# Performance work log

Measured on AMD Instinct MI355X. Metric: run time of the kernel, lower is better.

Reference implementation:

```python
import jax, jax.numpy as jnp
import numpy as np

NUM_HEADS = 4
GROUPS = 8
EPS = 1e-5


def setup_inputs() -> dict:
    key = jax.random.key(0)
    ks = jax.random.split(key, 8)
    B, C, H, W = 8, 512, 64, 64
    L, E = 77, 768
    std = 0.02
    return {
        "x": jax.random.normal(ks[0], (B, C, H, W), jnp.float32),
        "text_emb": jax.random.normal(ks[1], (B, L, E), jnp.float32),
        "attention_mask": jax.random.randint(ks[2], (B, L), 0, 2, jnp.int32),
        "Wq_w": jax.random.normal(ks[3], (C, C), jnp.float32) * std,
        "Wq_b": jnp.zeros((C,), jnp.float32),
        "Wk_w": jax.random.normal(ks[4], (C, E), jnp.float32) * std,
        "Wk_b": jnp.zeros((C,), jnp.float32),
        "Wv_w": jax.random.normal(ks[5], (C, E), jnp.float32) * std,
        "Wv_b": jnp.zeros((C,), jnp.float32),
        "gn_scale": jnp.ones((C,), jnp.float32),
        "gn_bias": jnp.zeros((C,), jnp.float32),
    }


def reference(x, text_emb, attention_mask, Wq_w, Wq_b, Wk_w, Wk_b, Wv_w, Wv_b, gn_scale, gn_bias):
    B, C, H, W = x.shape
    dh = C // NUM_HEADS
    scale = dh ** -0.5

    # [B, HW, C] queries from image features
    x_flat = x.reshape(B, C, H * W).transpose(0, 2, 1)
    Q = x_flat @ Wq_w.T + Wq_b                 # [B, S, C]
    K = text_emb @ Wk_w.T + Wk_b               # [B, L, C]
    V = text_emb @ Wv_w.T + Wv_b               # [B, L, C]

    def split_heads(t):
        Bt, T, _ = t.shape
        return t.reshape(Bt, T, NUM_HEADS, dh).transpose(0, 2, 1, 3)  # [B, h, T, dh]

    Qh, Kh, Vh = split_heads(Q), split_heads(K), split_heads(V)

    scores = jnp.einsum("bhqd,bhkd->bhqk", Qh, Kh) * scale  # [B, h, S, L]
    mask = (attention_mask == 0)[:, None, None, :]
    scores = jnp.where(mask, -jnp.inf, scores)
    probs = jax.nn.softmax(scores, axis=-1)
    # dropout layers are identity in eval mode
    attn = jnp.einsum("bhqk,bhkd->bhqd", probs, Vh)          # [B, h, S, dh]

    out = attn.transpose(0, 2, 1, 3).reshape(B, H * W, C)    # [B, S, C]
    out = out.transpose(0, 2, 1).reshape(B, C, H, W)

    # GroupNorm(8 groups, affine) over (C/G, H, W) per group
    g = out.reshape(B, GROUPS, -1)
    mean = g.mean(axis=-1, keepdims=True)
    var = g.var(axis=-1, keepdims=True)
    g = (g - mean) * jax.lax.rsqrt(var + EPS)
    out = g.reshape(B, C, H, W) * gn_scale[None, :, None, None] + gn_bias[None, :, None, None]
    return out
```

## Files before the change

### kernel.cpp

```cpp
#include <hip/hip_runtime.h>
#include <hip/hip_bf16.h>
#include <cstdint>


typedef __attribute__((ext_vector_type(8))) short short8;
typedef __attribute__((ext_vector_type(4))) short short4v;
typedef __attribute__((ext_vector_type(4))) float f32x4;

#define DEV __device__ __forceinline__

DEV float bf2f(unsigned short u){ union{uint32_t i; float f;} x; x.i = ((uint32_t)u) << 16; return x.f; }
DEV unsigned short f2bf(float f){ __hip_bfloat16 h = __float2bfloat16(f); return *reinterpret_cast<unsigned short*>(&h); }
DEV short8 ld8(const unsigned short* p){ return *reinterpret_cast<const short8*>(p); }
DEV f32x4 ldf4(const float* p){ return *reinterpret_cast<const f32x4*>(p); }

#if defined(__has_builtin)
#if __has_builtin(__builtin_amdgcn_global_load_lds)
#define HAVE_ASYNC_LDS 1
#endif
#endif

__global__ __launch_bounds__(256) void k_fat(const float* __restrict__ x,
                                             unsigned short* __restrict__ xTt,
                                             const float* __restrict__ text,
                                             const float* __restrict__ Wk,
                                             const float* __restrict__ Wkb,
                                             const float* __restrict__ Wv,
                                             const float* __restrict__ Wvb,
                                             unsigned short* __restrict__ wsK,
                                             unsigned short* __restrict__ wsVt,
                                             const float* __restrict__ Wq,
                                             unsigned short* __restrict__ wsWqT,
                                             int b0, int s_base, int slen, int SB){
  __shared__ unsigned short U[16896];
  const int tid = threadIdx.x;
  const int bx = blockIdx.x, by = blockIdx.y, bz = blockIdx.z;
  const int bg = b0 + bz;
  const int NT = slen >> 8;

  if (bx < NT){
    const int cc = by, c0 = cc * 64;
    const int s0 = s_base + bx * 256;
    {
      const int r = tid >> 2, sub = tid & 3;
      const float* src = &x[((size_t)(bg * 512 + c0 + r)) * 4096 + s0 + sub * 64];
      unsigned short* drow = &U[r * 264 + sub * 64];
      #pragma unroll
      for (int i = 0; i < 8; ++i){
        f32x4 a = ldf4(src + i * 8), b = ldf4(src + i * 8 + 4);
        short8 v;
        #pragma unroll
        for (int j = 0; j < 4; ++j){ v[j] = (short)f2bf(a[j]); v[j + 4] = (short)f2bf(b[j]); }
        *reinterpret_cast<short8*>(drow + i * 8) = v;
      }
    }
    __syncthreads();
    {
      const int j = tid;
      unsigned short v[64];
      #pragma unroll
      for (int r = 0; r < 64; ++r) v[r] = U[r * 264 + j];
      const int sloc = bx * 256 + j;
      unsigned short* dst = &xTt[(((size_t)bz * 8 + cc) * slen + sloc) * 64];
      #pragma unroll
      for (int g = 0; g < 8; ++g)
        *reinterpret_cast<short8*>(dst + g * 8) = *reinterpret_cast<short8*>(&v[g * 8]);
    }
  } else if (bx < NT + 2){
    unsigned short* At = U;
    unsigned short* Bt = U + 5760;
    const int wave = tid >> 6, lane = tid & 63;
    const int m16 = lane & 15, quad = lane >> 4;
    const int uc = (bx - NT) * 8 + by;
    const int u0 = uc * 64;
    const bool isK = (u0 < 512);
    const float* W  = isK ? Wk  : Wv;
    const float* Wb = isK ? Wkb : Wvb;
    const int c0 = u0 & 511;
    const int c  = c0 + wave * 16 + m16;
    f32x4 acc[5];
    #pragma unroll
    for (int mt = 0; mt < 5; ++mt) acc[mt] = (f32x4){0.f, 0.f, 0.f, 0.f};
    for (int kc = 0; kc < 12; ++kc){
      const int e0 = kc * 64;
      #pragma unroll
      for (int it = 0; it < 9; ++it){
        int slot = tid + it * 256;
        if (slot < 1280){
          int row = slot >> 4, e4 = (slot & 15) * 4;
          f32x4 v = (row < 77) ? ldf4(&text[((size_t)(bg * 77 + row)) * 768 + e0 + e4])
                               : (f32x4){0.f, 0.f, 0.f, 0.f};
          short4v o;
          #pragma unroll
          for (int j = 0; j < 4; ++j) o[j] = (short)f2bf(v[j]);
          *reinterpret_cast<short4v*>(&At[row * 72 + e4]) = o;
        } else {
          int bs = slot - 1280;
          int row = bs >> 4, e4 = (bs & 15) * 4;
          f32x4 v = ldf4(&W[((size_t)(c0 + row)) * 768 + e0 + e4]);
          short4v o;
          #pragma unroll
          for (int j = 0; j < 4; ++j) o[j] = (short)f2bf(v[j]);
          *reinterpret_cast<short4v*>(&Bt[row * 72 + e4]) = o;
        }
      }
      __syncthreads();
      #pragma unroll
      for (int kk = 0; kk < 64; kk += 32){
        short8 bf_ = *reinterpret_cast<const short8*>(&Bt[(wave * 16 + m16) * 72 + kk + quad * 8]);
        #pragma unroll
        for (int mt = 0; mt < 5; ++mt){
          short8 af_ = *reinterpret_cast<const short8*>(&At[(mt * 16 + m16) * 72 + kk + quad * 8]);
          acc[mt] = __builtin_amdgcn_mfma_f32_16x16x32_bf16(af_, bf_, acc[mt], 0, 0, 0);
        }
      }
      __syncthreads();
    }
    const float bias = Wb[c];
    if (isK){
      #pragma unroll
      for (int mt = 0; mt < 5; ++mt)
        #pragma unroll
        for (int r = 0; r < 4; ++r){
          int l = mt * 16 + quad * 4 + r;
          if (l < 77) wsK[((size_t)(bz * 77 + l)) * 512 + c] = f2bf(acc[mt][r] + bias);
        }
    } else {
      unsigned short* vr = &wsVt[((size_t)(bz * 512 + c)) * 96];
      #pragma unroll
      for (int mt = 0; mt < 5; ++mt){
        short4v pk;
        #pragma unroll
        for (int r = 0; r < 4; ++r) pk[r] = (short)f2bf(acc[mt][r] + bias);
        *reinterpret_cast<short4v*>(&vr[mt * 16 + quad * 4]) = pk;
      }
      short4v z = {};
      *reinterpret_cast<short4v*>(&vr[80 + quad * 4]) = z;
    }
  } else {
    unsigned short* t = U;
    const int nb = 8 * SB;
    const int p  = by + bz * 8;
    for (int tile = p; tile < 64; tile += nb){
      const int ti = tile >> 3, tj = tile & 7;
      #pragma unroll
      for (int it = 0; it < 2; ++it){
        int slot = tid + it * 256;
        int r = slot >> 3, sg = slot & 7;
        int sw = sg ^ (r >> 3);
        const float* src = &Wq[((size_t)(tj * 64 + r)) * 512 + ti * 64 + sg * 8];
        f32x4 a = ldf4(src), b2 = ldf4(src + 4);
        short8 v;
        #pragma unroll
        for (int j = 0; j < 4; ++j){ v[j] = (short)f2bf(a[j]); v[j + 4] = (short)f2bf(b2[j]); }
        *reinterpret_cast<short8*>(&t[r * 72 + sw * 8]) = v;
      }
      __syncthreads();
      #pragma unroll
      for (int it = 0; it < 2; ++it){
        int slot = tid + it * 256;
        int j = slot >> 3, i8 = slot & 7;
        short8 v;
        #pragma unroll
        for (int q = 0; q < 8; ++q){
          int dd = i8 * 8 + q;
          int sw = (j >> 3) ^ i8;
          v[q] = (short)t[dd * 72 + sw * 8 + (j & 7)];
        }
        *reinterpret_cast<short8*>(&wsWqT[((size_t)(ti * 64 + j)) * 512 + tj * 64 + i8 * 8]) = v;
      }
      __syncthreads();
    }
  }
}

__global__ __launch_bounds__(256) void k1b(const unsigned short* __restrict__ wsWqT,
                                           const unsigned short* __restrict__ wsK,
                                           const float* __restrict__ Wqb,
                                           unsigned short* __restrict__ wsKWq,
                                           float* __restrict__ kbias){
  const int tid = threadIdx.x;
  const int wave = tid >> 6, lane = tid & 63;
  const int m16 = lane & 15, quad = lane >> 4;
  const int cq = blockIdx.x, h = blockIdx.y, bz = blockIdx.z;
  const int cbase = cq * 128 + wave * 32;

  f32x4 acc[2][5];
  #pragma unroll
  for (int mt = 0; mt < 2; ++mt)
    #pragma unroll
    for (int nt = 0; nt < 5; ++nt) acc[mt][nt] = (f32x4){0.f, 0.f, 0.f, 0.f};

  #pragma unroll
  for (int ks = 0; ks < 4; ++ks){
    short8 aw[2];
    #pragma unroll
    for (int mt = 0; mt < 2; ++mt)
      aw[mt] = ld8(&wsWqT[(size_t)(cbase + mt * 16 + m16) * 512 + h * 128 + ks * 32 + quad * 8]);
    #pragma unroll
    for (int nt = 0; nt < 5; ++nt){
      int l = nt * 16 + m16;
      short8 bk = {};
      if (l < 77) bk = ld8(&wsK[((size_t)(bz * 77 + l)) * 512 + h * 128 + ks * 32 + quad * 8]);
      #pragma unroll
      for (int mt = 0; mt < 2; ++mt)
        acc[mt][nt] = __builtin_amdgcn_mfma_f32_16x16x32_bf16(aw[mt], bk, acc[mt][nt], 0, 0, 0);
    }
  }
  #pragma unroll
  for (int mt = 0; mt < 2; ++mt)
    #pragma unroll
    for (int nt = 0; nt < 5; ++nt){
      int l = nt * 16 + m16;
      short4v pk;
      #pragma unroll
      for (int r = 0; r < 4; ++r) pk[r] = (short)f2bf(acc[mt][nt][r]);
      *reinterpret_cast<short4v*>(&wsKWq[((size_t)((bz * 4 + h) * 80 + l)) * 512 + cbase + mt * 16 + quad * 4]) = pk;
    }
  if (cq == 0 && tid < 80){
    int l = tid;
    float kb = 0.f;
    if (l < 77){
      #pragma unroll
      for (int d = 0; d < 128; d += 8){
        short8 kv = ld8(&wsK[((size_t)(bz * 77 + l)) * 512 + h * 128 + d]);
        f32x4 wa = ldf4(&Wqb[h * 128 + d]);
        f32x4 wb = ldf4(&Wqb[h * 128 + d + 4]);
        #pragma unroll
        for (int j = 0; j < 4; ++j){
          kb += bf2f((unsigned short)kv[j]) * wa[j];
          kb += bf2f((unsigned short)kv[j + 4]) * wb[j];
        }
      }
    }
    kbias[(bz * 4 + h) * 80 + l] = kb;
  }
}

__global__ __launch_bounds__(256, 4) void k2_attn(const unsigned short* __restrict__ xTt,
                                                  const unsigned short* __restrict__ wsKWq,
                                                  const unsigned short* __restrict__ wsVt,
                                                  const int* __restrict__ amask,
                                                  const float* __restrict__ kbias,
                                                  float* __restrict__ out,
                                                  float* __restrict__ gnacc,
                                                  int b0, int s_base, int slen){
  __shared__ unsigned short arena[13312];
  __shared__ float maskf[96];
  unsigned short* Pt = arena;

  const int tid = threadIdx.x;
  const int wave = tid >> 6, lane = tid & 63;
  const int m16 = lane & 15, quad = lane >> 4;
  const int bz = blockIdx.x, h = blockIdx.y, st = blockIdx.z;
  const int bg = b0 + bz;
  const int s_glob = s_base + st * 128;
  const int R0 = (wave >> 1) * 64, C0 = (wave & 1) * 64;
  const int sw0 = wave * 32;
  const float scale = 0.08838834764831845f;

  if (tid < 96){
    int l = tid;
    float mbv = -30000.f;
    if (l < 77 && amask[bg * 77 + l] != 0) mbv = kbias[(bz * 4 + h) * 80 + l] * scale;
    maskf[l] = mbv;
  }

  const unsigned short* Abase = wsKWq + (size_t)((bz * 4 + h) * 80) * 512;
  const unsigned short* Bb    = xTt + (size_t)(bz * 8) * slen * 64;
  const int srow0 = st * 128 + sw0;

  f32x4 acc2[5][2];
  #pragma unroll
  for (int mt = 0; mt < 5; ++mt){ acc2[mt][0] = (f32x4){0.f,0.f,0.f,0.f}; acc2[mt][1] = (f32x4){0.f,0.f,0.f,0.f}; }

  auto stageA = [&](int kc, int buf){
    const int sbase = buf * 5120;
    #pragma unroll
    for (int it = 0; it < 3; ++it){
      const int ubase = it * 256 + wave * 64;
      if (ubase < 640){
        const int u = ubase + lane;
        int l = u >> 3, pos = (u & 7) ^ (l & 7);
        const unsigned short* src = Abase + (size_t)l * 512 + kc * 64 + pos * 8;
#ifdef HAVE_ASYNC_LDS
        __builtin_amdgcn_global_load_lds((const __attribute__((address_space(1))) void*)src,
                                         (__attribute__((address_space(3))) void*)&arena[sbase + ubase * 8],
                                         16, 0, 0);
#else
        *reinterpret_cast<short8*>(&arena[sbase + u * 8]) = ld8(src);
#endif
      }
    }
  };

  short8 Breg[2][4];
  auto loadB = [&](int kc, int buf){
    const unsigned short* Bc = Bb + ((size_t)kc * slen + srow0) * 64;
    #pragma unroll
    for (int nt = 0; nt < 2; ++nt)
      #pragma unroll
      for (int kk = 0; kk < 2; ++kk)
        Breg[buf][nt * 2 + kk] = ld8(&Bc[(size_t)(nt * 16 + m16) * 64 + kk * 32 + quad * 8]);
  };

  auto compute = [&](int buf){
    const int ab = buf * 5120;
    #pragma unroll
    for (int kk = 0; kk < 2; ++kk){
      short8 af[5];
      #pragma unroll
      for (int mt = 0; mt < 5; ++mt){
        int l = mt * 16 + m16;
        int p = (kk * 4 + quad) ^ (l & 7);
        af[mt] = *reinterpret_cast<const short8*>(&arena[ab + l * 64 + p * 8]);
      }
      #pragma unroll
      for (int mt = 0; mt < 5; ++mt)
        #pragma unroll
        for (int nt = 0; nt < 2; ++nt)
          acc2[mt][nt] = __builtin_amdgcn_mfma_f32_16x16x32_bf16(af[mt], Breg[buf][nt * 2 + kk], acc2[mt][nt], 0, 0, 0);
    }
  };

  stageA(0, 0);
  loadB(0, 0);
  __syncthreads();
  #pragma unroll
  for (int kc = 0; kc < 8; ++kc){
    if (kc < 7){ stageA(kc + 1, (kc + 1) & 1); loadB(kc + 1, (kc + 1) & 1); }
    compute(kc & 1);
    __syncthreads();
  }

  const unsigned short* Vb = wsVt + (size_t)(bz * 512 + h * 128) * 96;
  short8 av0[4];
  #pragma unroll
  for (int mt = 0; mt < 4; ++mt)
    av0[mt] = ld8(&Vb[(size_t)(R0 + mt * 16 + m16) * 96 + quad * 8]);

  {
    float mb[5][4];
    #pragma unroll
    for (int mt = 0; mt < 5; ++mt)
      #pragma unroll
      for (int r = 0; r < 4; ++r) mb[mt][r] = maskf[mt * 16 + quad * 4 + r];
    #pragma unroll
    for (int nt = 0; nt < 2; ++nt){
      float sv[5][4]; float mx = -3e38f;
      #pragma unroll
      for (int mt = 0; mt < 5; ++mt)
        #pragma unroll
        for (int r = 0; r < 4; ++r){
          float v = acc2[mt][nt][r] * scale + mb[mt][r];
          sv[mt][r] = v; mx = fmaxf(mx, v);
        }
      mx = fmaxf(mx, __shfl_xor(mx, 16)); mx = fmaxf(mx, __shfl_xor(mx, 32));
      float sum = 0.f;
      #pragma unroll
      for (int mt = 0; mt < 5; ++mt)
        #pragma unroll
        for (int r = 0; r < 4; ++r){ float e = __expf(sv[mt][r] - mx); sv[mt][r] = e; sum += e; }
      sum += __shfl_xor(sum, 16); sum += __shfl_xor(sum, 32);
      float inv = 1.0f / sum;
      int sl = sw0 + nt * 16 + m16;
      #pragma unroll
      for (int mt = 0; mt < 5; ++mt){
        short4v pk;
        #pragma unroll
        for (int r = 0; r < 4; ++r) pk[r] = (short)f2bf(sv[mt][r] * inv);
        *reinterpret_cast<short4v*>(&Pt[sl * 104 + mt * 16 + quad * 4]) = pk;
      }
      short4v z = {};
      *reinterpret_cast<short4v*>(&Pt[sl * 104 + 80 + quad * 4]) = z;
    }
  }
  __syncthreads();

  f32x4 acc3[4][4];
  #pragma unroll
  for (int mt = 0; mt < 4; ++mt)
    #pragma unroll
    for (int nt = 0; nt < 4; ++nt) acc3[mt][nt] = (f32x4){0.f, 0.f, 0.f, 0.f};
  #pragma unroll
  for (int ks = 0; ks < 3; ++ks){
    short8 av[4], bp[4];
    #pragma unroll
    for (int mt = 0; mt < 4; ++mt)
      av[mt] = (ks == 0) ? av0[mt]
                         : ld8(&Vb[(size_t)(R0 + mt * 16 + m16) * 96 + ks * 32 + quad * 8]);
    #pragma unroll
    for (int nt = 0; nt < 4; ++nt)
      bp[nt] = *reinterpret_cast<const short8*>(&Pt[(C0 + nt * 16 + m16) * 104 + ks * 32 + quad * 8]);
    #pragma unroll
    for (int mt = 0; mt < 4; ++mt)
      #pragma unroll
      for (int nt = 0; nt < 4; ++nt)
        acc3[mt][nt] = __builtin_amdgcn_mfma_f32_16x16x32_bf16(av[mt], bp[nt], acc3[mt][nt], 0, 0, 0);
  }
  float sum = 0.f, ssq = 0.f;
  #pragma unroll
  for (int mt = 0; mt < 4; ++mt)
    #pragma unroll
    for (int nt = 0; nt < 4; ++nt){
      int sidx = s_glob + C0 + nt * 16 + m16;
      #pragma unroll
      for (int r = 0; r < 4; ++r){
        float v = acc3[mt][nt][r];
        sum += v; ssq += v * v;
        int d = h * 128 + R0 + mt * 16 + quad * 4 + r;
        out[(size_t)(bg * 512 + d) * 4096 + sidx] = v;
      }
    }
  #pragma unroll
  for (int off = 1; off < 64; off <<= 1){ sum += __shfl_xor(sum, off); ssq += __shfl_xor(ssq, off); }
  if (lane == 0){
    int g = h * 2 + (R0 >> 6);
    atomicAdd(&gnacc[(bg * 8 + g) * 2],     sum);
    atomicAdd(&gnacc[(bg * 8 + g) * 2 + 1], ssq);
  }
}

__global__ __launch_bounds__(256) void k3_gn(float* __restrict__ out,
                                             const float* __restrict__ gnacc,
                                             const float* __restrict__ gns,
                                             const float* __restrict__ gnb){
  const int bx = blockIdx.x;
  const int b = bx >> 9, c = bx & 511;
  const int g = c >> 6;
  const float s  = gnacc[(b * 8 + g) * 2];
  const float ss = gnacc[(b * 8 + g) * 2 + 1];
  const float invN = 1.f / 262144.f;
  const float mean = s * invN;
  const float var  = ss * invN - mean * mean;
  const float rstd = rsqrtf(fmaxf(var, 0.f) + 1e-5f);
  const float a  = rstd * gns[c];
  const float bb = gnb[c] - mean * a;
  const size_t base = (size_t)bx * 4096;
  #pragma unroll
  for (int p = 0; p < 4; ++p){
    size_t off = base + p * 1024 + threadIdx.x * 4;
    f32x4 v = ldf4(&out[off]);
    f32x4 o;
    #pragma unroll
    for (int j = 0; j < 4; ++j) o[j] = v[j] * a + bb;
    *reinterpret_cast<f32x4*>(&out[off]) = o;
  }
}

extern "C" void kernel_launch(void* const* d_in, const int* in_sizes, int n_in,
                              void* d_out, int out_size, void* d_ws, size_t ws_size,
                              hipStream_t stream){
  (void)in_sizes; (void)n_in; (void)out_size;
  const float* x    = (const float*)d_in[0];
  const float* text = (const float*)d_in[1];
  const int*   am   = (const int*)d_in[2];
  const float* Wq   = (const float*)d_in[3];
  const float* Wqb  = (const float*)d_in[4];
  const float* Wk   = (const float*)d_in[5];
  const float* Wkb  = (const float*)d_in[6];
  const float* Wv   = (const float*)d_in[7];
  const float* Wvb  = (const float*)d_in[8];
  const float* gns  = (const float*)d_in[9];
  const float* gnb  = (const float*)d_in[10];
  float* out = (float*)d_out;

  auto need = [](int SB, int SLEN) -> size_t {
    return 512ull + 524288ull + (size_t)SB * 506112ull + (size_t)SB * SLEN * 1024ull;
  };
  int SB = 8, SLEN = 4096;
  if      (ws_size >= need(8, 4096)) { SB = 8; SLEN = 4096; }
  else if (ws_size >= need(4, 4096)) { SB = 4; SLEN = 4096; }
  else if (ws_size >= need(2, 4096)) { SB = 2; SLEN = 4096; }
  else if (ws_size >= need(1, 4096)) { SB = 1; SLEN = 4096; }
  else if (ws_size >= need(1, 1024)) { SB = 1; SLEN = 1024; }
  else                               { SB = 1; SLEN = 256;  }

  uint8_t* ws = (uint8_t*)d_ws;
  float*          gnacc = (float*)ws;
  unsigned short* wsWqT = (unsigned short*)(ws + 512);
  unsigned short* wsK   = wsWqT + 512 * 512;
  unsigned short* wsVt  = wsK  + (size_t)SB * 77 * 512;
  unsigned short* wsKWq = wsVt + (size_t)SB * 512 * 96;
  float*          kbias = (float*)(wsKWq + (size_t)SB * 4 * 80 * 512);
  unsigned short* xTt   = (unsigned short*)(kbias + (size_t)SB * 4 * 80);

  hipMemsetAsync(gnacc, 0, 128 * sizeof(float), stream);
  for (int b0 = 0; b0 < 8; b0 += SB){
    for (int s_base = 0; s_base < 4096; s_base += SLEN){
      const int NT = SLEN >> 8;
      k_fat<<<dim3(NT + 3, 8, SB), 256, 0, stream>>>(x, xTt, text, Wk, Wkb, Wv, Wvb,
                                                     wsK, wsVt, Wq, wsWqT, b0, s_base, SLEN, SB);
      if (s_base == 0)
        k1b<<<dim3(4, 4, SB), 256, 0, stream>>>(wsWqT, wsK, Wqb, wsKWq, kbias);
      k2_attn<<<dim3(SB, 4, SLEN / 128), 256, 0, stream>>>(xTt, wsKWq, wsVt, am, kbias,
                                                           out, gnacc, b0, s_base, SLEN);
    }
  }
  k3_gn<<<4096, 256, 0, stream>>>(out, gnacc, gns, gnb);
}
```

Measured before the change: 132.2 us.

## Prefetch K/V GEMM tiles into registers and schedule GEMM blocks first in k_fat

Inside k_fat, the K/V projection blocks now issue the global loads for the next 64-wide K chunk into registers before the MFMA work on the current chunk. This overlaps load latency with compute instead of leaving the load-convert-store sequence exposed on every iteration. Block order changes so the GEMM blocks (bx<2) and the Wq transpose block (bx==2) come before the x-transpose blocks, so the longer-running blocks start earliest. The x and Wq transposes also issue all their vector loads up front, and the Wq LDS tile drops its XOR swizzle, which may bring back LDS bank conflicts on the column reads.

```diff
diff --git a/kernel.cpp b/kernel.cpp
--- a/kernel.cpp
+++ b/kernel.cpp
@@ -36,21 +36,23 @@
   const int tid = threadIdx.x;
   const int bx = blockIdx.x, by = blockIdx.y, bz = blockIdx.z;
   const int bg = b0 + bz;
-  const int NT = slen >> 8;
-
-  if (bx < NT){
+
+  if (bx >= 3){
     const int cc = by, c0 = cc * 64;
-    const int s0 = s_base + bx * 256;
+    const int tile = bx - 3;
+    const int s0 = s_base + tile * 256;
     {
       const int r = tid >> 2, sub = tid & 3;
       const float* src = &x[((size_t)(bg * 512 + c0 + r)) * 4096 + s0 + sub * 64];
+      f32x4 rv[16];
+      #pragma unroll
+      for (int i = 0; i < 16; ++i) rv[i] = ldf4(src + i * 4);
       unsigned short* drow = &U[r * 264 + sub * 64];
       #pragma unroll
       for (int i = 0; i < 8; ++i){
-        f32x4 a = ldf4(src + i * 8), b = ldf4(src + i * 8 + 4);
         short8 v;
         #pragma unroll
-        for (int j = 0; j < 4; ++j){ v[j] = (short)f2bf(a[j]); v[j + 4] = (short)f2bf(b[j]); }
+        for (int j = 0; j < 4; ++j){ v[j] = (short)f2bf(rv[2*i][j]); v[j + 4] = (short)f2bf(rv[2*i+1][j]); }
         *reinterpret_cast<short8*>(drow + i * 8) = v;
       }
     }
@@ -60,51 +62,63 @@
       unsigned short v[64];
       #pragma unroll
       for (int r = 0; r < 64; ++r) v[r] = U[r * 264 + j];
-      const int sloc = bx * 256 + j;
+      const int sloc = tile * 256 + j;
       unsigned short* dst = &xTt[(((size_t)bz * 8 + cc) * slen + sloc) * 64];
       #pragma unroll
       for (int g = 0; g < 8; ++g)
         *reinterpret_cast<short8*>(dst + g * 8) = *reinterpret_cast<short8*>(&v[g * 8]);
     }
-  } else if (bx < NT + 2){
+  } else if (bx < 2){
     unsigned short* At = U;
     unsigned short* Bt = U + 5760;
     const int wave = tid >> 6, lane = tid & 63;
     const int m16 = lane & 15, quad = lane >> 4;
-    const int uc = (bx - NT) * 8 + by;
+    const int uc = bx * 8 + by;
     const int u0 = uc * 64;
     const bool isK = (u0 < 512);
     const float* W  = isK ? Wk  : Wv;
     const float* Wb = isK ? Wkb : Wvb;
     const int c0 = u0 & 511;
     const int c  = c0 + wave * 16 + m16;
+
+    int srow[9], se4[9]; bool sA[9], sval[9];
+    #pragma unroll
+    for (int it = 0; it < 9; ++it){
+      int slot = tid + it * 256;
+      if (slot < 1280){ sA[it] = true;  srow[it] = slot >> 4;          se4[it] = (slot & 15) * 4; sval[it] = (srow[it] < 77); }
+      else            { sA[it] = false; srow[it] = (slot - 1280) >> 4; se4[it] = ((slot - 1280) & 15) * 4; sval[it] = true; }
+    }
+    f32x4 preg[9];
+    auto issue = [&](int kc){
+      const int e0 = kc * 64;
+      #pragma unroll
+      for (int it = 0; it < 9; ++it){
+        if (sA[it])
+          preg[it] = sval[it] ? ldf4(&text[((size_t)(bg * 77 + srow[it])) * 768 + e0 + se4[it]])
+                              : (f32x4){0.f, 0.f, 0.f, 0.f};
+        else
+          preg[it] = ldf4(&W[((size_t)(c0 + srow[it])) * 768 + e0 + se4[it]]);
+      }
+    };
+    auto write_lds = [&](){
+      #pragma unroll
+      for (int it = 0; it < 9; ++it){
+        short4v o;
+        #pragma unroll
+        for (int j = 0; j < 4; ++j) o[j] = (short)f2bf(preg[it][j]);
+        if (sA[it]) *reinterpret_cast<short4v*>(&At[srow[it] * 72 + se4[it]]) = o;
+        else        *reinterpret_cast<short4v*>(&Bt[srow[it] * 72 + se4[it]]) = o;
+      }
+    };
+
     f32x4 acc[5];
     #pragma unroll
     for (int mt = 0; mt < 5; ++mt) acc[mt] = (f32x4){0.f, 0.f, 0.f, 0.f};
+    issue(0);
     for (int kc = 0; kc < 12; ++kc){
-      const int e0 = kc * 64;
-      #pragma unroll
-      for (int it = 0; it < 9; ++it){
-        int slot = tid + it * 256;
-        if (slot < 1280){
-          int row = slot >> 4, e4 = (slot & 15) * 4;
-          f32x4 v = (row < 77) ? ldf4(&text[((size_t)(bg * 77 + row)) * 768 + e0 + e4])
-                               : (f32x4){0.f, 0.f, 0.f, 0.f};
-          short4v o;
-          #pragma unroll
-          for (int j = 0; j < 4; ++j) o[j] = (short)f2bf(v[j]);
-          *reinterpret_cast<short4v*>(&At[row * 72 + e4]) = o;
-        } else {
-          int bs = slot - 1280;
-          int row = bs >> 4, e4 = (bs & 15) * 4;
-          f32x4 v = ldf4(&W[((size_t)(c0 + row)) * 768 + e0 + e4]);
-          short4v o;
-          #pragma unroll
-          for (int j = 0; j < 4; ++j) o[j] = (short)f2bf(v[j]);
-          *reinterpret_cast<short4v*>(&Bt[row * 72 + e4]) = o;
-        }
-      }
+      write_lds();
       __syncthreads();
+      if (kc < 11) issue(kc + 1);
       #pragma unroll
       for (int kk = 0; kk < 64; kk += 32){
         short8 bf_ = *reinterpret_cast<const short8*>(&Bt[(wave * 16 + m16) * 72 + kk + quad * 8]);
@@ -143,17 +157,20 @@
     const int p  = by + bz * 8;
     for (int tile = p; tile < 64; tile += nb){
       const int ti = tile >> 3, tj = tile & 7;
-      #pragma unroll
-      for (int it = 0; it < 2; ++it){
-        int slot = tid + it * 256;
-        int r = slot >> 3, sg = slot & 7;
-        int sw = sg ^ (r >> 3);
-        const float* src = &Wq[((size_t)(tj * 64 + r)) * 512 + ti * 64 + sg * 8];
-        f32x4 a = ldf4(src), b2 = ldf4(src + 4);
-        short8 v;
-        #pragma unroll
-        for (int j = 0; j < 4; ++j){ v[j] = (short)f2bf(a[j]); v[j + 4] = (short)f2bf(b2[j]); }
-        *reinterpret_cast<short8*>(&t[r * 72 + sw * 8]) = v;
+      {
+        const int r = tid >> 2, sub = tid & 3;
+        const float* src = &Wq[((size_t)(tj * 64 + r)) * 512 + ti * 64 + sub * 16];
+        f32x4 rv[4];
+        #pragma unroll
+        for (int i = 0; i < 4; ++i) rv[i] = ldf4(src + i * 4);
+        unsigned short* drow = &t[r * 72 + sub * 16];
+        #pragma unroll
+        for (int i = 0; i < 2; ++i){
+          short8 v;
+          #pragma unroll
+          for (int j = 0; j < 4; ++j){ v[j] = (short)f2bf(rv[2*i][j]); v[j + 4] = (short)f2bf(rv[2*i+1][j]); }
+          *reinterpret_cast<short8*>(drow + i * 8) = v;
+        }
       }
       __syncthreads();
       #pragma unroll
@@ -162,11 +179,8 @@
         int j = slot >> 3, i8 = slot & 7;
         short8 v;
         #pragma unroll
-        for (int q = 0; q < 8; ++q){
-          int dd = i8 * 8 + q;
-          int sw = (j >> 3) ^ i8;
-          v[q] = (short)t[dd * 72 + sw * 8 + (j & 7)];
-        }
+        for (int q = 0; q < 8; ++q)
+          v[q] = (short)t[(i8 * 8 + q) * 72 + (j & 63)];
         *reinterpret_cast<short8*>(&wsWqT[((size_t)(ti * 64 + j)) * 512 + tj * 64 + i8 * 8]) = v;
       }
       __syncthreads();
```

Result: faster. 117.9 us (-10.8%).
